# Kernel tuning notes

Hardware: AMD Instinct MI355X
Metric: run time of the kernel (lower is better)

Reference implementation:

```python
import jax, jax.numpy as jnp
from jax import lax
import numpy as np

B, T, I, H, C = 32, 256, 128, 128, 100


def setup_inputs() -> dict:
    key = jax.random.key(0)
    ks = jax.random.split(key, 9)
    s = 1.0 / np.sqrt(H)  # PyTorch LSTMCell init range
    inp = {
        "x": jax.random.normal(ks[0], (B, T, I), dtype=jnp.float32),
        "w_ih": jax.random.uniform(ks[1], (4 * H, I), jnp.float32, -s, s),
        "b_ih": jax.random.uniform(ks[2], (4 * H,), jnp.float32, -s, s),
        "w_hh": jax.random.uniform(ks[3], (4 * H, H), jnp.float32, -s, s),
        "b_hh": jax.random.uniform(ks[4], (4 * H,), jnp.float32, -s, s),
        # attention params: normal(mean=0, std=0.01) per the source
        "w1": 0.01 * jax.random.normal(ks[5], (2 * H, H), dtype=jnp.float32),
        "w2": 0.01 * jax.random.normal(ks[6], (H, 1), dtype=jnp.float32),
        "w_fc": jax.random.uniform(ks[7], (C, H), jnp.float32, -s, s),
        "b_fc": jax.random.uniform(ks[8], (C,), jnp.float32, -s, s),
    }
    return inp


def _forward(x, w_ih, b_ih, w_hh, b_hh, w1, w2, w_fc, b_fc):
    Bv, Tv, _ = x.shape
    Hv = w_hh.shape[1]
    h0 = jnp.zeros((Bv, Hv), x.dtype)
    c0 = jnp.zeros((Bv, Hv), x.dtype)
    # memory buffer: slot 0 holds the initial zero hidden state (as in the
    # torch code, h_old starts as h_t=0); slots 1..T filled as we go.
    # Unwritten (future) slots are zero, so their attn contribution
    # attn_w * h_old is exactly zero -> no mask needed, matching the
    # growing-memory semantics of the original loop.
    mem0 = jnp.zeros((Bv, Tv + 1, Hv), x.dtype)
    attn0 = jnp.zeros((Bv, Hv), x.dtype)

    def step(carry, inp):
        h, c, mem, _ = carry
        x_t, i = inp
        # PyTorch LSTMCell: gate order i, f, g, o
        gates = x_t @ w_ih.T + b_ih + h @ w_hh.T + b_hh
        ig, fg, gg, og = jnp.split(gates, 4, axis=-1)
        c = jax.nn.sigmoid(fg) * c + jax.nn.sigmoid(ig) * jnp.tanh(gg)
        h = jax.nn.sigmoid(og) * jnp.tanh(c)
        # additive attention scores over the memory (NO softmax in source)
        h_rep = jnp.broadcast_to(h[:, None, :], mem.shape)  # [B, T+1, H]
        cat = jnp.concatenate([h_rep, mem], axis=-1)        # [B, T+1, 2H]
        s = jnp.tanh(cat @ w1) @ w2                          # [B, T+1, 1]
        attn_c = jnp.sum(s * mem, axis=1)                    # [B, H]
        mem = mem.at[:, i + 1, :].set(h)  # append h_t to memory
        return (h, c, mem, attn_c), None

    xs = (jnp.transpose(x, (1, 0, 2)), jnp.arange(Tv))
    (h, c, mem, attn_c), _ = lax.scan(step, (h0, c0, mem0, attn0), xs)
    return (h + attn_c) @ w_fc.T + b_fc


def reference(x, w_ih, b_ih, w_hh, b_hh, w1, w2, w_fc, b_fc):
    return _forward(x, w_ih, b_ih, w_hh, b_hh, w1, w2, w_fc, b_fc)
```

## Files before the change

kernel.cpp:

```cpp
#include <hip/hip_runtime.h>
#include <hip/hip_bf16.h>


#define Bsz 32
#define Tsz 256
#define Isz 128
#define Hsz 128
#define Csz 100
#define G4H 512

typedef short v8s __attribute__((ext_vector_type(8)));
typedef float v4fa __attribute__((ext_vector_type(4)));

__device__ __forceinline__ float2 pk_fma(float2 a, float2 b, float2 c) {
    float2 d;
    asm("v_pk_fma_f32 %0, %1, %2, %3" : "=v"(d) : "v"(a), "v"(b), "v"(c));
    return d;
}
__device__ __forceinline__ float quad_rsum(float x) {
    int t = __builtin_amdgcn_update_dpp(0, __float_as_int(x), 0xB1, 0xF, 0xF, true);
    x += __int_as_float(t);
    t = __builtin_amdgcn_update_dpp(0, __float_as_int(x), 0x4E, 0xF, 0xF, true);
    x += __int_as_float(t);
    return x;
}
__device__ __forceinline__ float rcpf(float x) { return __builtin_amdgcn_rcpf(x); }
__device__ __forceinline__ float sigm_n(float x) { return rcpf(1.0f + __expf(-x)); }
__device__ __forceinline__ float tanh_n(float x) {
    float ax = fabsf(x);
    float e = __expf(-2.0f * ax);
    float t = (1.0f - e) * rcpf(1.0f + e);
    return copysignf(t, x);
}
__device__ __forceinline__ float tanh_s(float x) { return tanh_n(x); }

__global__ __launch_bounds__(256) void prep_kernel(
    const float* __restrict__ w_ih, const float* __restrict__ b_ih,
    const float* __restrict__ w_hh, const float* __restrict__ b_hh,
    const float* __restrict__ w1,
    __hip_bfloat16* __restrict__ W2ih, __hip_bfloat16* __restrict__ W2v,
    float* __restrict__ whh_pk, float* __restrict__ bias) {
    int idx = blockIdx.x * blockDim.x + threadIdx.x;
    if (idx < G4H * Isz) {
        int n = idx >> 7;
        int k = idx & 127;
        float x = w_ih[idx];
        __hip_bfloat16 hi = __float2bfloat16(x);
        __hip_bfloat16 lo = __float2bfloat16(x - __bfloat162float(hi));
        W2ih[(size_t)n * 384 + k] = hi;
        W2ih[(size_t)n * 384 + 128 + k] = lo;
        W2ih[(size_t)n * 384 + 256 + k] = hi;

        int j4  = idx & 3;
        int q   = (idx >> 2) & 3;
        int d   = (idx >> 4) & 127;
        int gi  = (idx >> 11) & 3;
        int kk4 = (idx >> 13) & 7;
        whh_pk[idx] = w_hh[(size_t)((gi << 7) + d) * 128 + (q << 5) + (kk4 << 2) + j4];
    }
    if (idx < Hsz * Hsz) {
        int n = idx >> 7;
        int k = idx & 127;
        float x = w1[(size_t)(128 + k) * Hsz + n];
        __hip_bfloat16 hi = __float2bfloat16(x);
        __hip_bfloat16 lo = __float2bfloat16(x - __bfloat162float(hi));
        W2v[(size_t)n * 384 + k] = hi;
        W2v[(size_t)n * 384 + 128 + k] = lo;
        W2v[(size_t)n * 384 + 256 + k] = hi;
    }
    if (idx < G4H) bias[idx] = b_ih[idx] + b_hh[idx];
}

__global__ __launch_bounds__(256) void split256(
    const float* __restrict__ src, __hip_bfloat16* __restrict__ dst, int total) {
    int i = blockIdx.x * 256 + threadIdx.x;
    if (i >= total) return;
    int m = i >> 7, k = i & 127;
    float x = src[i];
    __hip_bfloat16 hi = __float2bfloat16(x);
    dst[(size_t)m * 256 + k] = hi;
    dst[(size_t)m * 256 + 128 + k] = __float2bfloat16(x - __bfloat162float(hi));
}

__global__ __launch_bounds__(256) void gemm_mfma(
    const __hip_bfloat16* __restrict__ A2, const __hip_bfloat16* __restrict__ W2,
    const float* __restrict__ bias, float* __restrict__ C, int M, int N) {
    const int tid = threadIdx.x;
    const int w = tid >> 6, lane = tid & 63;
    const int m0 = blockIdx.y * 64 + (w & 1) * 32;
    const int n0 = blockIdx.x * 64 + (w >> 1) * 32;
    const int r = lane & 15, quad = lane >> 4;

    v4fa acc[2][2] = {};
    const short* Ab = (const short*)A2;
    const short* Wb = (const short*)W2;

    #pragma unroll
    for (int ks = 0; ks < 12; ++ks) {
        int ka = (ks & 3) * 32 + ((ks >= 8) ? 128 : 0) + quad * 8;
        int kb = ks * 32 + quad * 8;
        v8s a0 = *(const v8s*)(Ab + (size_t)(m0 + r) * 256 + ka);
        v8s a1 = *(const v8s*)(Ab + (size_t)(m0 + 16 + r) * 256 + ka);
        v8s b0 = *(const v8s*)(Wb + (size_t)(n0 + r) * 384 + kb);
        v8s b1 = *(const v8s*)(Wb + (size_t)(n0 + 16 + r) * 384 + kb);
        acc[0][0] = __builtin_amdgcn_mfma_f32_16x16x32_bf16(a0, b0, acc[0][0], 0, 0, 0);
        acc[0][1] = __builtin_amdgcn_mfma_f32_16x16x32_bf16(a0, b1, acc[0][1], 0, 0, 0);
        acc[1][0] = __builtin_amdgcn_mfma_f32_16x16x32_bf16(a1, b0, acc[1][0], 0, 0, 0);
        acc[1][1] = __builtin_amdgcn_mfma_f32_16x16x32_bf16(a1, b1, acc[1][1], 0, 0, 0);
    }
    #pragma unroll
    for (int i = 0; i < 2; ++i)
        #pragma unroll
        for (int j = 0; j < 2; ++j) {
            int cn = n0 + 16 * j + r;
            float bb = bias ? bias[cn] : 0.0f;
            #pragma unroll
            for (int rr = 0; rr < 4; ++rr) {
                int row = m0 + 16 * i + quad * 4 + rr;
                C[(size_t)row * N + cn] = acc[i][j][rr] + bb;
            }
        }
}

#define HPAD(k) ((k) + 8 * ((k) >> 5))

__global__ __launch_bounds__(512, 2) void lstm_seq(
    const float* __restrict__ G, const float* __restrict__ whh_pk,
    float* __restrict__ H_all) {
    const int b = blockIdx.x;
    const int tid = threadIdx.x;
    const int d = tid >> 2;
    const int q = tid & 3;

    __shared__ float h_s[2][160];

    float2 w2v[4][16];
    {
        const float4* wp = (const float4*)whh_pk;
        #pragma unroll
        for (int kk4 = 0; kk4 < 8; ++kk4)
            #pragma unroll
            for (int gi = 0; gi < 4; ++gi) {
                float4 v = wp[((kk4 * 4 + gi) * 128 + d) * 4 + q];
                w2v[gi][kk4 * 2]     = make_float2(v.x, v.y);
                w2v[gi][kk4 * 2 + 1] = make_float2(v.z, v.w);
            }
    }

    if (tid < 320) ((float*)h_s)[tid] = 0.0f;
    float c = 0.0f;
    __syncthreads();

    const float* Gq = G + (size_t)b * Tsz * G4H + q * 128 + d;
    float* Hst = H_all + (size_t)b * Tsz * Hsz + d;

    float gval = Gq[0];
    int cur = 0;
    for (int t = 0; t < Tsz; ++t) {
        const int tn = (t < Tsz - 1) ? t + 1 : t;
        float ngval = Gq[(size_t)tn * G4H];

        float2 accA[4], accB[4];
        #pragma unroll
        for (int gi = 0; gi < 4; ++gi) {
            accA[gi] = make_float2(q == gi ? gval : 0.f, 0.f);
            accB[gi] = make_float2(0.f, 0.f);
        }
        const float4* hb4 = (const float4*)&h_s[cur][q * 40];
        #pragma unroll
        for (int kk4 = 0; kk4 < 8; ++kk4) {
            float4 h4 = hb4[kk4];
            float2 hA = make_float2(h4.x, h4.y);
            float2 hB = make_float2(h4.z, h4.w);
            accA[0] = pk_fma(hA, w2v[0][2 * kk4], accA[0]);
            accA[1] = pk_fma(hA, w2v[1][2 * kk4], accA[1]);
            accA[2] = pk_fma(hA, w2v[2][2 * kk4], accA[2]);
            accA[3] = pk_fma(hA, w2v[3][2 * kk4], accA[3]);
            accB[0] = pk_fma(hB, w2v[0][2 * kk4 + 1], accB[0]);
            accB[1] = pk_fma(hB, w2v[1][2 * kk4 + 1], accB[1]);
            accB[2] = pk_fma(hB, w2v[2][2 * kk4 + 1], accB[2]);
            accB[3] = pk_fma(hB, w2v[3][2 * kk4 + 1], accB[3]);
        }
        float a0 = quad_rsum(accA[0].x + accA[0].y + accB[0].x + accB[0].y);
        float a1 = quad_rsum(accA[1].x + accA[1].y + accB[1].x + accB[1].y);
        float a2 = quad_rsum(accA[2].x + accA[2].y + accB[2].x + accB[2].y);
        float a3 = quad_rsum(accA[3].x + accA[3].y + accB[3].x + accB[3].y);

        float iv = sigm_n(a0);
        float fv = sigm_n(a1);
        float gv = tanh_n(a2);
        float ov = sigm_n(a3);
        c = fv * c + iv * gv;
        float h = ov * tanh_n(c);

        if (q == 0) {
            h_s[cur ^ 1][HPAD(d)] = h;
            Hst[(size_t)t * Hsz] = h;
        }
        gval = ngval;
        __syncthreads();
        cur ^= 1;
    }
}

__global__ __launch_bounds__(256) void attn_out(
    const float* __restrict__ H_all, const float* __restrict__ KV,
    const float* __restrict__ w1, const float* __restrict__ w2,
    const float* __restrict__ w_fc, const float* __restrict__ b_fc,
    float* __restrict__ out) {
    int b = blockIdx.x;
    int tid = threadIdx.x;
    __shared__ float hT[Hsz];
    __shared__ float q_s[Hsz];
    __shared__ float w2s[Hsz];
    __shared__ float s_s[Tsz];
    __shared__ float r2[2][Hsz];
    __shared__ float r_s[Hsz];

    const float* Hb = H_all + (size_t)b * Tsz * Hsz;
    const float* KVb = KV + (size_t)b * Tsz * Hsz;

    if (tid < Hsz) {
        hT[tid] = Hb[255 * Hsz + tid];
        w2s[tid] = w2[tid];
    }
    __syncthreads();
    if (tid < Hsz) {
        float acc = 0.f;
        #pragma unroll 8
        for (int k = 0; k < Hsz; ++k) acc = fmaf(hT[k], w1[k * Hsz + tid], acc);
        q_s[tid] = acc;
    }
    __syncthreads();

    const int qd = tid >> 2, ql = tid & 3;
    #pragma unroll
    for (int jj = 0; jj < 4; ++jj) {
        int j = qd + jj * 64;
        float p = 0.f;
        if (j < 255) {
            const float* kv = KVb + (size_t)j * Hsz + ql * 32;
            const float* qs = q_s + ql * 32;
            const float* wv = w2s + ql * 32;
            #pragma unroll 8
            for (int k = 0; k < 32; ++k)
                p = fmaf(tanh_s(qs[k] + kv[k]), wv[k], p);
        }
        p = quad_rsum(p);
        if (ql == 0 && j < 255) s_s[j] = p;
    }
    __syncthreads();

    {
        int dd = tid & 127, half = tid >> 7;
        int j0 = half * 128, je = half ? 255 : 128;
        float acc = 0.f;
        #pragma unroll 4
        for (int j = j0; j < je; ++j) acc = fmaf(s_s[j], Hb[(size_t)j * Hsz + dd], acc);
        r2[half][dd] = acc;
    }
    __syncthreads();
    if (tid < Hsz) r_s[tid] = hT[tid] + r2[0][tid] + r2[1][tid];
    __syncthreads();

    {
        int o = tid >> 1, half = tid & 1;
        float acc = 0.f;
        if (o < Csz) {
            const float* wr = w_fc + (size_t)o * Hsz + half * 64;
            const float* rr = r_s + half * 64;
            #pragma unroll 8
            for (int k = 0; k < 64; ++k) acc = fmaf(rr[k], wr[k], acc);
        }
        acc += __shfl_xor(acc, 1);
        if (half == 0 && o < Csz) out[b * Csz + o] = acc + b_fc[o];
    }
}

extern "C" void kernel_launch(void* const* d_in, const int* in_sizes, int n_in,
                              void* d_out, int out_size, void* d_ws, size_t ws_size,
                              hipStream_t stream) {
    const float* x    = (const float*)d_in[0];
    const float* w_ih = (const float*)d_in[1];
    const float* b_ih = (const float*)d_in[2];
    const float* w_hh = (const float*)d_in[3];
    const float* b_hh = (const float*)d_in[4];
    const float* w1   = (const float*)d_in[5];
    const float* w2   = (const float*)d_in[6];
    const float* w_fc = (const float*)d_in[7];
    const float* b_fc = (const float*)d_in[8];

    float* ws = (float*)d_ws;
    float* whh_pk = ws;
    float* bias   = whh_pk + 65536;
    __hip_bfloat16* W2ih = (__hip_bfloat16*)(bias + 512);
    __hip_bfloat16* W2v  = (__hip_bfloat16*)(bias + 512 + 98304);
    __hip_bfloat16* x2   = (__hip_bfloat16*)(bias + 512 + 98304 + 24576);
    float* G      = bias + 512 + 98304 + 24576 + 1048576;
    __hip_bfloat16* H2 = (__hip_bfloat16*)G;
    float* KV     = G + 2097152;
    float* H_all  = G + 4194304;

    prep_kernel<<<256, 256, 0, stream>>>(w_ih, b_ih, w_hh, b_hh, w1,
                                         W2ih, W2v, whh_pk, bias);

    split256<<<4096, 256, 0, stream>>>(x, x2, Bsz * Tsz * Isz);

    dim3 gG(G4H / 64, (Bsz * Tsz) / 64);
    gemm_mfma<<<gG, 256, 0, stream>>>(x2, W2ih, bias, G, Bsz * Tsz, G4H);

    lstm_seq<<<Bsz, 512, 0, stream>>>(G, whh_pk, H_all);

    split256<<<4096, 256, 0, stream>>>(H_all, H2, Bsz * Tsz * Hsz);

    dim3 gK(Hsz / 64, (Bsz * Tsz) / 64);
    gemm_mfma<<<gK, 256, 0, stream>>>(H2, W2v, nullptr, KV, Bsz * Tsz, Hsz);

    attn_out<<<Bsz, 256, 0, stream>>>(H_all, KV, w1, w2, w_fc, b_fc, (float*)d_out);
}
```

Measured before the change: 340.8 us.

## Fuse bf16 split into GEMM loads and split attention across time tiles

The GEMM now reads fp32 activations directly and does the hi/lo bf16 split in registers, which removes the two separate split256 kernels and their intermediate buffers. The attention tail is also split into a scores kernel over 4 time tiles per batch that accumulates partial context with atomics, followed by a small fc kernel. This adds parallelism to the previously 32-block attention pass, at the cost of an extra launch and non-deterministic atomic summation order.

```diff
diff --git a/kernel.cpp b/kernel.cpp
--- a/kernel.cpp
+++ b/kernel.cpp
@@ -33,13 +33,21 @@
     return copysignf(t, x);
 }
 __device__ __forceinline__ float tanh_s(float x) { return tanh_n(x); }
+__device__ __forceinline__ short bf16_bits(float x) {
+    __hip_bfloat16 h = __float2bfloat16(x);
+    return *reinterpret_cast<short*>(&h);
+}
+__device__ __forceinline__ float bf16_val(float x) {
+    return __bfloat162float(__float2bfloat16(x));
+}
 
 __global__ __launch_bounds__(256) void prep_kernel(
     const float* __restrict__ w_ih, const float* __restrict__ b_ih,
     const float* __restrict__ w_hh, const float* __restrict__ b_hh,
     const float* __restrict__ w1,
     __hip_bfloat16* __restrict__ W2ih, __hip_bfloat16* __restrict__ W2v,
-    float* __restrict__ whh_pk, float* __restrict__ bias) {
+    float* __restrict__ whh_pk, float* __restrict__ bias,
+    float* __restrict__ attn_c) {
     int idx = blockIdx.x * blockDim.x + threadIdx.x;
     if (idx < G4H * Isz) {
         int n = idx >> 7;
@@ -69,21 +77,11 @@
         W2v[(size_t)n * 384 + 256 + k] = hi;
     }
     if (idx < G4H) bias[idx] = b_ih[idx] + b_hh[idx];
-}
-
-__global__ __launch_bounds__(256) void split256(
-    const float* __restrict__ src, __hip_bfloat16* __restrict__ dst, int total) {
-    int i = blockIdx.x * 256 + threadIdx.x;
-    if (i >= total) return;
-    int m = i >> 7, k = i & 127;
-    float x = src[i];
-    __hip_bfloat16 hi = __float2bfloat16(x);
-    dst[(size_t)m * 256 + k] = hi;
-    dst[(size_t)m * 256 + 128 + k] = __float2bfloat16(x - __bfloat162float(hi));
-}
-
-__global__ __launch_bounds__(256) void gemm_mfma(
-    const __hip_bfloat16* __restrict__ A2, const __hip_bfloat16* __restrict__ W2,
+    if (idx < Bsz * Hsz) attn_c[idx] = 0.0f;
+}
+
+__global__ __launch_bounds__(256) void gemm_mfma_f32a(
+    const float* __restrict__ A, const __hip_bfloat16* __restrict__ W2,
     const float* __restrict__ bias, float* __restrict__ C, int M, int N) {
     const int tid = threadIdx.x;
     const int w = tid >> 6, lane = tid & 63;
@@ -91,16 +89,34 @@
     const int n0 = blockIdx.x * 64 + (w >> 1) * 32;
     const int r = lane & 15, quad = lane >> 4;
 
+    v8s Ahi[2][4], Alo[2][4];
+    #pragma unroll
+    for (int i = 0; i < 2; ++i)
+        #pragma unroll
+        for (int cb = 0; cb < 4; ++cb) {
+            const float* src = A + (size_t)(m0 + 16 * i + r) * Isz + cb * 32 + quad * 8;
+            float4 f0 = *(const float4*)src;
+            float4 f1 = *(const float4*)(src + 4);
+            float f[8] = {f0.x, f0.y, f0.z, f0.w, f1.x, f1.y, f1.z, f1.w};
+            v8s hi, lo;
+            #pragma unroll
+            for (int e = 0; e < 8; ++e) {
+                float hv = bf16_val(f[e]);
+                hi[e] = bf16_bits(f[e]);
+                lo[e] = bf16_bits(f[e] - hv);
+            }
+            Ahi[i][cb] = hi;
+            Alo[i][cb] = lo;
+        }
+
     v4fa acc[2][2] = {};
-    const short* Ab = (const short*)A2;
     const short* Wb = (const short*)W2;
-
     #pragma unroll
     for (int ks = 0; ks < 12; ++ks) {
-        int ka = (ks & 3) * 32 + ((ks >= 8) ? 128 : 0) + quad * 8;
+        int cb = ks & 3;
+        v8s a0 = (ks >= 8) ? Alo[0][cb] : Ahi[0][cb];
+        v8s a1 = (ks >= 8) ? Alo[1][cb] : Ahi[1][cb];
         int kb = ks * 32 + quad * 8;
-        v8s a0 = *(const v8s*)(Ab + (size_t)(m0 + r) * 256 + ka);
-        v8s a1 = *(const v8s*)(Ab + (size_t)(m0 + 16 + r) * 256 + ka);
         v8s b0 = *(const v8s*)(Wb + (size_t)(n0 + r) * 384 + kb);
         v8s b1 = *(const v8s*)(Wb + (size_t)(n0 + 16 + r) * 384 + kb);
         acc[0][0] = __builtin_amdgcn_mfma_f32_16x16x32_bf16(a0, b0, acc[0][0], 0, 0, 0);
@@ -203,19 +219,17 @@
     }
 }
 
-__global__ __launch_bounds__(256) void attn_out(
+__global__ __launch_bounds__(256) void scores_part(
     const float* __restrict__ H_all, const float* __restrict__ KV,
     const float* __restrict__ w1, const float* __restrict__ w2,
-    const float* __restrict__ w_fc, const float* __restrict__ b_fc,
-    float* __restrict__ out) {
-    int b = blockIdx.x;
-    int tid = threadIdx.x;
+    float* __restrict__ attn_c) {
+    const int b = blockIdx.y, jt = blockIdx.x;
+    const int tid = threadIdx.x;
     __shared__ float hT[Hsz];
     __shared__ float q_s[Hsz];
     __shared__ float w2s[Hsz];
-    __shared__ float s_s[Tsz];
-    __shared__ float r2[2][Hsz];
-    __shared__ float r_s[Hsz];
+    __shared__ float s_s[64];
+    __shared__ float part[2][Hsz];
 
     const float* Hb = H_all + (size_t)b * Tsz * Hsz;
     const float* KVb = KV + (size_t)b * Tsz * Hsz;
@@ -233,48 +247,55 @@
     }
     __syncthreads();
 
-    const int qd = tid >> 2, ql = tid & 3;
-    #pragma unroll
-    for (int jj = 0; jj < 4; ++jj) {
-        int j = qd + jj * 64;
-        float p = 0.f;
-        if (j < 255) {
-            const float* kv = KVb + (size_t)j * Hsz + ql * 32;
-            const float* qs = q_s + ql * 32;
-            const float* wv = w2s + ql * 32;
-            #pragma unroll 8
-            for (int k = 0; k < 32; ++k)
-                p = fmaf(tanh_s(qs[k] + kv[k]), wv[k], p);
-        }
-        p = quad_rsum(p);
-        if (ql == 0 && j < 255) s_s[j] = p;
-    }
+    const int jl = tid >> 2, ql = tid & 3;
+    const int j = jt * 64 + jl;
+    float p = 0.f;
+    if (j < 255) {
+        const float* kv = KVb + (size_t)j * Hsz + ql * 32;
+        const float* qs = q_s + ql * 32;
+        const float* wv = w2s + ql * 32;
+        #pragma unroll 8
+        for (int k = 0; k < 32; ++k)
+            p = fmaf(tanh_s(qs[k] + kv[k]), wv[k], p);
+    }
+    p = quad_rsum(p);
+    if (ql == 0) s_s[jl] = (j < 255) ? p : 0.0f;
     __syncthreads();
 
     {
-        int dd = tid & 127, half = tid >> 7;
-        int j0 = half * 128, je = half ? 255 : 128;
+        const int dd = tid & 127, half = tid >> 7;
         float acc = 0.f;
         #pragma unroll 4
-        for (int j = j0; j < je; ++j) acc = fmaf(s_s[j], Hb[(size_t)j * Hsz + dd], acc);
-        r2[half][dd] = acc;
-    }
-    __syncthreads();
-    if (tid < Hsz) r_s[tid] = hT[tid] + r2[0][tid] + r2[1][tid];
-    __syncthreads();
-
-    {
-        int o = tid >> 1, half = tid & 1;
-        float acc = 0.f;
-        if (o < Csz) {
-            const float* wr = w_fc + (size_t)o * Hsz + half * 64;
-            const float* rr = r_s + half * 64;
-            #pragma unroll 8
-            for (int k = 0; k < 64; ++k) acc = fmaf(rr[k], wr[k], acc);
-        }
-        acc += __shfl_xor(acc, 1);
-        if (half == 0 && o < Csz) out[b * Csz + o] = acc + b_fc[o];
-    }
+        for (int u = 0; u < 32; ++u) {
+            int lj = half * 32 + u;
+            int jj = jt * 64 + lj;
+            if (jj < 255) acc = fmaf(s_s[lj], Hb[(size_t)jj * Hsz + dd], acc);
+        }
+        part[half][dd] = acc;
+    }
+    __syncthreads();
+    if (tid < Hsz) atomicAdd(&attn_c[b * Hsz + tid], part[0][tid] + part[1][tid]);
+}
+
+__global__ __launch_bounds__(256) void fc_out(
+    const float* __restrict__ H_all, const float* __restrict__ attn_c,
+    const float* __restrict__ w_fc, const float* __restrict__ b_fc,
+    float* __restrict__ out) {
+    const int b = blockIdx.x, tid = threadIdx.x;
+    __shared__ float r_s[Hsz];
+    if (tid < Hsz)
+        r_s[tid] = H_all[(size_t)b * Tsz * Hsz + 255 * Hsz + tid] + attn_c[b * Hsz + tid];
+    __syncthreads();
+    const int o = tid >> 1, half = tid & 1;
+    float acc = 0.f;
+    if (o < Csz) {
+        const float* wr = w_fc + (size_t)o * Hsz + half * 64;
+        const float* rr = r_s + half * 64;
+        #pragma unroll 8
+        for (int k = 0; k < 64; ++k) acc = fmaf(rr[k], wr[k], acc);
+    }
+    acc += __shfl_xor(acc, 1);
+    if (half == 0 && o < Csz) out[b * Csz + o] = acc + b_fc[o];
 }
 
 extern "C" void kernel_launch(void* const* d_in, const int* in_sizes, int n_in,
@@ -293,28 +314,26 @@
     float* ws = (float*)d_ws;
     float* whh_pk = ws;
     float* bias   = whh_pk + 65536;
-    __hip_bfloat16* W2ih = (__hip_bfloat16*)(bias + 512);
-    __hip_bfloat16* W2v  = (__hip_bfloat16*)(bias + 512 + 98304);
-    __hip_bfloat16* x2   = (__hip_bfloat16*)(bias + 512 + 98304 + 24576);
-    float* G      = bias + 512 + 98304 + 24576 + 1048576;
-    __hip_bfloat16* H2 = (__hip_bfloat16*)G;
-    float* KV     = G + 2097152;
+    float* attn_c = bias + 512;
+    __hip_bfloat16* W2ih = (__hip_bfloat16*)(attn_c + 4096);
+    __hip_bfloat16* W2v  = (__hip_bfloat16*)(attn_c + 4096 + 98304);
+    float* G      = attn_c + 4096 + 98304 + 24576;
     float* H_all  = G + 4194304;
+    float* KV     = H_all + 1048576;
 
     prep_kernel<<<256, 256, 0, stream>>>(w_ih, b_ih, w_hh, b_hh, w1,
-                                         W2ih, W2v, whh_pk, bias);
-
-    split256<<<4096, 256, 0, stream>>>(x, x2, Bsz * Tsz * Isz);
+                                         W2ih, W2v, whh_pk, bias, attn_c);
 
     dim3 gG(G4H / 64, (Bsz * Tsz) / 64);
-    gemm_mfma<<<gG, 256, 0, stream>>>(x2, W2ih, bias, G, Bsz * Tsz, G4H);
+    gemm_mfma_f32a<<<gG, 256, 0, stream>>>(x, W2ih, bias, G, Bsz * Tsz, G4H);
 
     lstm_seq<<<Bsz, 512, 0, stream>>>(G, whh_pk, H_all);
 
-    split256<<<4096, 256, 0, stream>>>(H_all, H2, Bsz * Tsz * Hsz);
-
     dim3 gK(Hsz / 64, (Bsz * Tsz) / 64);
-    gemm_mfma<<<gK, 256, 0, stream>>>(H2, W2v, nullptr, KV, Bsz * Tsz, Hsz);
-
-    attn_out<<<Bsz, 256, 0, stream>>>(H_all, KV, w1, w2, w_fc, b_fc, (float*)d_out);
-}
+    gemm_mfma_f32a<<<gK, 256, 0, stream>>>(H_all, W2v, nullptr, KV, Bsz * Tsz, Hsz);
+
+    dim3 gS(4, Bsz);
+    scores_part<<<gS, 256, 0, stream>>>(H_all, KV, w1, w2, attn_c);
+
+    fc_out<<<Bsz, 256, 0, stream>>>(H_all, attn_c, w_fc, b_fc, (float*)d_out);
+}
```

After: 330.7 us. 1.03x faster.
